# Performance work log

Measured on AMD Instinct MI355X. Metric: run time of the kernel, lower is better.

The kernel has to match this reference:

```python
import jax, jax.numpy as jnp
import numpy as np

B, S, D, H = 2, 2048, 1024, 16
HD = D // H
EPS = 1e-5

def _ln(x, g, b):
    mu = jnp.mean(x, axis=-1, keepdims=True)
    var = jnp.var(x, axis=-1, keepdims=True)
    return (x - mu) * jax.lax.rsqrt(var + EPS) * g + b

def setup_inputs() -> dict:
    key = jax.random.key(0)
    ks = jax.random.split(key, 6)
    sc = lambda n: 1.0 / np.sqrt(n)
    return {
        "x": jax.random.normal(ks[0], (B, S, D), jnp.float32),
        "W_qkv": jax.random.normal(ks[1], (D, 3 * D), jnp.float32) * sc(D),
        "b_qkv": jnp.zeros((3 * D,), jnp.float32),
        "W_o": jax.random.normal(ks[2], (D, D), jnp.float32) * sc(D),
        "b_o": jnp.zeros((D,), jnp.float32),
        "W_fc": jax.random.normal(ks[3], (D, 4 * D), jnp.float32) * sc(D),
        "b_fc": jnp.zeros((4 * D,), jnp.float32),
        "W_pr": jax.random.normal(ks[4], (4 * D, D), jnp.float32) * sc(4 * D),
        "b_pr": jnp.zeros((D,), jnp.float32),
        "g1": jnp.ones((D,), jnp.float32),
        "beta1": jnp.zeros((D,), jnp.float32),
        "g2": jnp.ones((D,), jnp.float32),
        "beta2": jnp.zeros((D,), jnp.float32),
    }

def reference(x, W_qkv, b_qkv, W_o, b_o, W_fc, b_fc, W_pr, b_pr, g1, beta1, g2, beta2):
    # pre-norm attention
    h = _ln(x, g1, beta1)
    qkv = h @ W_qkv + b_qkv                      # [B,S,3D]
    q, k, v = jnp.split(qkv, 3, axis=-1)
    q = q.reshape(B, S, H, HD).transpose(0, 2, 1, 3)  # [B,H,S,hd]
    k = k.reshape(B, S, H, HD).transpose(0, 2, 1, 3)
    v = v.reshape(B, S, H, HD).transpose(0, 2, 1, 3)
    scores = jnp.einsum('bhqd,bhkd->bhqk', q, k) / np.sqrt(HD)
    causal = jnp.tril(jnp.ones((S, S), bool))
    scores = jnp.where(causal, scores, -jnp.inf)
    attn = jax.nn.softmax(scores, axis=-1)
    out = jnp.einsum('bhqk,bhkd->bhqd', attn, v)
    out = out.transpose(0, 2, 1, 3).reshape(B, S, D)
    x = x + out @ W_o + b_o
    # pre-norm MLP (exact erf GELU, matching torch F.gelu default)
    h2 = _ln(x, g2, beta2)
    h2 = jax.nn.gelu(h2 @ W_fc + b_fc, approximate=False)
    x = x + h2 @ W_pr + b_pr
    return x
```

## Files before the change

### kernel.cpp

```cpp
#include <hip/hip_runtime.h>
#include <cstdint>
#include <cstddef>

#define Bb 2
#define Ss 2048
#define Dd 1024
#define Hh 16

typedef __attribute__((ext_vector_type(8))) short short8;
typedef __attribute__((ext_vector_type(4))) short short4v;
typedef __attribute__((ext_vector_type(4))) float float4v;

__device__ inline short f2bf(float f) {
  unsigned u = __builtin_bit_cast(unsigned, f);
  u = (u + 0x7fffu + ((u >> 16) & 1u)) >> 16;
  return (short)u;
}

__device__ inline float bf2f(short s) {
  unsigned u = ((unsigned)(unsigned short)s) << 16;
  return __builtin_bit_cast(float, u);
}

__device__ inline unsigned cvt_pk_bf16(float lo, float hi) {
  unsigned r;
  asm("v_cvt_pk_bf16_f32 %0, %1, %2" : "=v"(r) : "v"(lo), "v"(hi));
  return r;
}

__device__ inline void gl_lds16(const void* g, void* l) {
  __builtin_amdgcn_global_load_lds(
      (__attribute__((address_space(1))) void*)(void*)(g),
      (__attribute__((address_space(3))) void*)(l), 16, 0, 0);
}

#define MFMA(a, b, c) __builtin_amdgcn_mfma_f32_16x16x32_bf16((a), (b), (c), 0, 0, 0)

__device__ __forceinline__ void ln_row(const float* __restrict__ x,
                                       const float* __restrict__ g,
                                       const float* __restrict__ be,
                                       short* __restrict__ out, int row,
                                       float* red) {
  int tid = threadIdx.x;
  const float4* xr = (const float4*)(x + (size_t)row * Dd);
  float4 v = xr[tid];
  float s = v.x + v.y + v.z + v.w;
  float q = v.x * v.x + v.y * v.y + v.z * v.z + v.w * v.w;
#pragma unroll
  for (int off = 1; off < 64; off <<= 1) {
    s += __shfl_xor(s, off);
    q += __shfl_xor(q, off);
  }
  int w = tid >> 6;
  if ((tid & 63) == 0) { red[w] = s; red[4 + w] = q; }
  __syncthreads();
  s = red[0] + red[1] + red[2] + red[3];
  q = red[4] + red[5] + red[6] + red[7];
  float mu = s * (1.0f / Dd);
  float var = q * (1.0f / Dd) - mu * mu;
  float rstd = rsqrtf(var + 1e-5f);
  float4 gv = ((const float4*)g)[tid], bv = ((const float4*)be)[tid];
  short4v o;
  o.x = f2bf((v.x - mu) * rstd * gv.x + bv.x);
  o.y = f2bf((v.y - mu) * rstd * gv.y + bv.y);
  o.z = f2bf((v.z - mu) * rstd * gv.z + bv.z);
  o.w = f2bf((v.w - mu) * rstd * gv.w + bv.w);
  *(short4v*)(out + (size_t)row * Dd + tid * 4) = o;
}

__global__ __launch_bounds__(256) void prep_kernel(
    const float* __restrict__ W0, short* __restrict__ T0,
    const float* __restrict__ W1, short* __restrict__ T1,
    const float* __restrict__ W2, short* __restrict__ T2,
    const float* __restrict__ W3, short* __restrict__ T3,
    const float* __restrict__ x, const float* __restrict__ g1,
    const float* __restrict__ be1, short* __restrict__ h1) {
  __shared__ __align__(16) float t[32][33];
  int id = blockIdx.x;
  if (id >= 12288) {
    ln_row(x, g1, be1, h1, id - 12288, &t[0][0]);
    return;
  }
  const float* W; short* Wt; int N, K, tix;
  if (id < 3072)      { W = W0; Wt = T0; N = 3072; K = 1024; tix = id; }
  else if (id < 4096) { W = W1; Wt = T1; N = 1024; K = 1024; tix = id - 3072; }
  else if (id < 8192) { W = W2; Wt = T2; N = 4096; K = 1024; tix = id - 4096; }
  else                { W = W3; Wt = T3; N = 1024; K = 4096; tix = id - 8192; }
  int nx = N / 32;
  int n0 = (tix % nx) * 32, k0 = (tix / nx) * 32;
  int tx = threadIdx.x & 31, ty = threadIdx.x >> 5;
#pragma unroll
  for (int i = 0; i < 4; i++)
    t[ty + 8 * i][tx] = W[(size_t)(k0 + ty + 8 * i) * N + n0 + tx];
  __syncthreads();
#pragma unroll
  for (int i = 0; i < 4; i++)
    Wt[(size_t)(n0 + ty + 8 * i) * K + k0 + tx] = f2bf(t[tx][ty + 8 * i]);
}

__global__ __launch_bounds__(256) void reduce_ln_kernel(const float* __restrict__ x,
                                                        const float* __restrict__ bias,
                                                        const short* __restrict__ parts,
                                                        const float* __restrict__ g,
                                                        const float* __restrict__ be,
                                                        float* __restrict__ x1,
                                                        short* __restrict__ h2) {
  int row = blockIdx.x, tid = threadIdx.x;
  size_t base = (size_t)row * Dd + tid * 4;
  float4 v = *(const float4*)(x + base);
  float4 bv = ((const float4*)bias)[tid];
  v.x += bv.x; v.y += bv.y; v.z += bv.z; v.w += bv.w;
#pragma unroll
  for (int s = 0; s < 2; s++) {
    short4v p = *(const short4v*)(parts + (size_t)s * 4096 * Dd + base);
    v.x += bf2f(p.x); v.y += bf2f(p.y); v.z += bf2f(p.z); v.w += bf2f(p.w);
  }
  *(float4*)(x1 + base) = v;
  float s = v.x + v.y + v.z + v.w;
  float q = v.x * v.x + v.y * v.y + v.z * v.z + v.w * v.w;
#pragma unroll
  for (int off = 1; off < 64; off <<= 1) {
    s += __shfl_xor(s, off);
    q += __shfl_xor(q, off);
  }
  __shared__ float as_[4], aq_[4];
  int w = tid >> 6;
  if ((tid & 63) == 0) { as_[w] = s; aq_[w] = q; }
  __syncthreads();
  s = as_[0] + as_[1] + as_[2] + as_[3];
  q = aq_[0] + aq_[1] + aq_[2] + aq_[3];
  float mu = s * (1.0f / Dd);
  float var = q * (1.0f / Dd) - mu * mu;
  float rstd = rsqrtf(var + 1e-5f);
  float4 gv = ((const float4*)g)[tid], b2 = ((const float4*)be)[tid];
  short4v o;
  o.x = f2bf((v.x - mu) * rstd * gv.x + b2.x);
  o.y = f2bf((v.y - mu) * rstd * gv.y + b2.y);
  o.z = f2bf((v.z - mu) * rstd * gv.z + b2.z);
  o.w = f2bf((v.w - mu) * rstd * gv.w + b2.w);
  *(short4v*)(h2 + base) = o;
}

__global__ __launch_bounds__(256) void reduce_kernel(const float* __restrict__ src,
                                                     const float* __restrict__ bias,
                                                     const short* __restrict__ parts,
                                                     float* __restrict__ dst) {
  int row = blockIdx.x, tid = threadIdx.x;
  size_t base = (size_t)row * Dd + tid * 4;
  float4 v = *(const float4*)(src + base);
  float4 bv = ((const float4*)bias)[tid];
  v.x += bv.x; v.y += bv.y; v.z += bv.z; v.w += bv.w;
#pragma unroll
  for (int s = 0; s < 2; s++) {
    short4v p = *(const short4v*)(parts + (size_t)s * 4096 * Dd + base);
    v.x += bf2f(p.x); v.y += bf2f(p.y); v.z += bf2f(p.z); v.w += bf2f(p.w);
  }
  *(float4*)(dst + base) = v;
}

template <int MODE>
__device__ __forceinline__ void gemm_tile(const short* __restrict__ A,
                                          const short* __restrict__ Bt,
                                          const float* __restrict__ bias,
                                          void* __restrict__ outp,
                                          short* __restrict__ vtp,
                                          int M, int N, int K,
                                          int m0, int n0, int zp,
                                          int ks, int ke, char* smem) {
  short* As = (short*)smem;
  short* Bs = (short*)smem + 128 * 64;
  const int tid = threadIdx.x;
  const int w = tid >> 6, lane = tid & 63;
  const int sr = lane >> 3;
  const int sc = lane & 7;
  const int gc = sc ^ sr;
  const int fr = lane & 15;
  const int g = lane >> 4;
  const int wm = (w >> 1) * 64, wn = (w & 1) * 64;
  float4v acc[4][4] = {};
  const short* Ag = A + (size_t)(m0 + w * 32 + sr) * K + gc * 8;
  const short* Bg = Bt + (size_t)(n0 + w * 32 + sr) * K + gc * 8;
  short* Asw = As + (w * 32 + sr) * 64 + sc * 8;
  short* Bsw = Bs + (w * 32 + sr) * 64 + sc * 8;
#pragma unroll
  for (int i = 0; i < 4; i++) {
    gl_lds16(Ag + (size_t)(i * 8) * K + ks, Asw + i * 8 * 64);
    gl_lds16(Bg + (size_t)(i * 8) * K + ks, Bsw + i * 8 * 64);
  }
  for (int k0 = ks; k0 < ke; k0 += 64) {
    __syncthreads();
    short8 a[2][4], b[2][4];
#pragma unroll
    for (int kh = 0; kh < 2; kh++) {
#pragma unroll
      for (int i = 0; i < 4; i++) {
        int row = wm + i * 16 + fr;
        int slot = (g + kh * 4) ^ (row & 7);
        a[kh][i] = *(const short8*)(As + row * 64 + slot * 8);
      }
#pragma unroll
      for (int j = 0; j < 4; j++) {
        int row = wn + j * 16 + fr;
        int slot = (g + kh * 4) ^ (row & 7);
        b[kh][j] = *(const short8*)(Bs + row * 64 + slot * 8);
      }
    }
    __syncthreads();
    if (k0 + 64 < ke) {
#pragma unroll
      for (int i = 0; i < 4; i++) {
        gl_lds16(Ag + (size_t)(i * 8) * K + k0 + 64, Asw + i * 8 * 64);
        gl_lds16(Bg + (size_t)(i * 8) * K + k0 + 64, Bsw + i * 8 * 64);
      }
    }
#pragma unroll
    for (int kh = 0; kh < 2; kh++)
#pragma unroll
      for (int i = 0; i < 4; i++)
#pragma unroll
        for (int j = 0; j < 4; j++)
          acc[i][j] = MFMA(a[kh][i], b[kh][j], acc[i][j]);
  }
  const int crow = g * 4;
  const int ccol = fr;
#pragma unroll
  for (int i = 0; i < 4; i++) {
#pragma unroll
    for (int j = 0; j < 4; j++) {
      int col = n0 + wn + j * 16 + ccol;
      float bcol = (MODE == 3) ? 0.f : bias[col];
      short sh[4];
#pragma unroll
      for (int r = 0; r < 4; r++) {
        int row = m0 + wm + i * 16 + crow + r;
        float v = acc[i][j][r] + bcol;
        if (MODE == 4) {
          if (col < 1024) v *= 0.18033688f;
          sh[r] = f2bf(v);
          ((short*)outp)[(size_t)row * N + col] = sh[r];
        } else if (MODE == 2) {
          float y = 0.79788456f * (v + 0.044715f * v * v * v);
          float e = __builtin_amdgcn_exp2f(y * 2.885390082f);
          float th = 1.0f - 2.0f * __builtin_amdgcn_rcpf(e + 1.0f);
          v = 0.5f * v * (1.0f + th);
          ((short*)outp)[(size_t)row * N + col] = f2bf(v);
        } else {
          short* pp = (short*)outp + (size_t)zp * M * N;
          pp[(size_t)row * N + col] = f2bf(v);
        }
      }
      if (MODE == 4 && col >= 2048) {
        int hd = col - 2048;
        int rbase = m0 + wm + i * 16 + crow;
        int bq = rbase >> 11, sb = rbase & 2047;
        int bh = bq * 16 + (hd >> 6), d = hd & 63;
        short4v pk;
        pk.x = sh[0]; pk.y = sh[1]; pk.z = sh[2]; pk.w = sh[3];
        *(short4v*)(vtp + (size_t)(bh * 64 + d) * Ss + sb) = pk;
      }
    }
  }
}

__global__ __launch_bounds__(256) void k_gemm_qkv(const short* __restrict__ A,
                                                  const short* __restrict__ Bt,
                                                  const float* __restrict__ bias,
                                                  short* __restrict__ o,
                                                  short* __restrict__ Vt) {
  __shared__ __align__(16) char smem[32768];
  int t = blockIdx.x;
  int c8 = t & 7, tt = t >> 3;
  int m0 = ((c8 >> 1) * 8 + tt / 12) * 128;
  int n0 = ((c8 & 1) * 12 + tt % 12) * 128;
  gemm_tile<4>(A, Bt, bias, o, Vt, 4096, 3072, 1024, m0, n0, 0, 0, 1024, smem);
}

__global__ __launch_bounds__(256) void k_gemm_fc(const short* __restrict__ A,
                                                 const short* __restrict__ Bt,
                                                 const float* __restrict__ bias,
                                                 short* __restrict__ o) {
  __shared__ __align__(16) char smem[32768];
  int t = blockIdx.x;
  int c8 = t & 7, tt = t >> 3;
  int m0 = ((c8 >> 1) * 8 + tt / 16) * 128;
  int n0 = ((c8 & 1) * 16 + tt % 16) * 128;
  gemm_tile<2>(A, Bt, bias, o, nullptr, 4096, 4096, 1024, m0, n0, 0, 0, 1024, smem);
}

__global__ __launch_bounds__(256) void k_gemm_wo(const short* __restrict__ A,
                                                 const short* __restrict__ Bt,
                                                 short* __restrict__ parts) {
  __shared__ __align__(16) char smem[32768];
  int c = blockIdx.x;
  int z = c >> 8, rem = c & 255;
  int c8 = rem & 7, tt = rem >> 3;
  int m0 = (c8 * 4 + tt / 8) * 128, n0 = (tt % 8) * 128;
  gemm_tile<3>(A, Bt, nullptr, parts, nullptr, 4096, 1024, 1024, m0, n0, z,
               z * 512, z * 512 + 512, smem);
}

__global__ __launch_bounds__(256) void k_gemm_pr(const short* __restrict__ A,
                                                 const short* __restrict__ Bt,
                                                 short* __restrict__ parts) {
  __shared__ __align__(16) char smem[32768];
  int c = blockIdx.x;
  int z = c >> 8, rem = c & 255;
  int c8 = rem & 7, tt = rem >> 3;
  int m0 = (c8 * 4 + tt / 8) * 128, n0 = (tt % 8) * 128;
  gemm_tile<3>(A, Bt, nullptr, parts, nullptr, 4096, 1024, 4096, m0, n0, z,
               z * 2048, z * 2048 + 2048, smem);
}

__global__ __launch_bounds__(256) void flash_kernel(const short* __restrict__ qkv,
                                                    const short* __restrict__ Vt,
                                                    short* __restrict__ att) {
  __shared__ __align__(16) short Ks[4096];
  __shared__ __align__(16) short Vs[4096];
  __shared__ __align__(16) short P[4][16 * 72];
  const int w = threadIdx.x >> 6, lane = threadIdx.x & 63;
  const int qb = 31 - (blockIdx.x >> 5);
  const int bh = blockIdx.x & 31;
  const int b = bh >> 4, h = bh & 15;
  const int qbase = qb * 64 + w * 16;
  const int q = lane & 15;
  const int g = lane >> 4;
  const int fk = g * 8;
  short* Pw = &P[w][0];

  const int L0 = w * 64 + lane, L1 = L0 + 256;
  const int r0 = L0 >> 3, c0 = (L0 & 7) ^ (r0 & 7);
  const int r1 = L1 >> 3, c1 = (L1 & 7) ^ (r1 & 7);
  const short* kg0 = qkv + (size_t)(b * Ss + r0) * 3072 + 1024 + h * 64 + c0 * 8;
  const short* kg1 = qkv + (size_t)(b * Ss + r1) * 3072 + 1024 + h * 64 + c1 * 8;
  const short* vg0 = Vt + (size_t)(bh * 64 + r0) * Ss + c0 * 8;
  const short* vg1 = Vt + (size_t)(bh * 64 + r1) * Ss + c1 * 8;

  short8 qf[2];
  {
    const short* qrow = qkv + (size_t)(b * Ss + qbase + q) * 3072 + h * 64;
    qf[0] = *(const short8*)(qrow + fk);
    qf[1] = *(const short8*)(qrow + 32 + fk);
  }
  float4v o[4] = {};
  float l_i = 0.f;
  const int nkt = qb + 1;

  gl_lds16(kg0, Ks + L0 * 8);
  gl_lds16(kg1, Ks + L1 * 8);
  gl_lds16(vg0, Vs + L0 * 8);
  gl_lds16(vg1, Vs + L1 * 8);

  for (int kt = 0; kt < nkt; kt++) {
    const int kbase = kt * 64;
    __syncthreads();

    short8 kf[4][2], vf[4][2];
#pragma unroll
    for (int t = 0; t < 4; t++) {
      const int row = 16 * t + q;
      const int sw = (g ^ (row & 7)) * 8;
      kf[t][0] = *(const short8*)(Ks + row * 64 + sw);
      kf[t][1] = *(const short8*)(Ks + row * 64 + (sw ^ 32));
      vf[t][0] = *(const short8*)(Vs + row * 64 + sw);
      vf[t][1] = *(const short8*)(Vs + row * 64 + (sw ^ 32));
    }
    __syncthreads();
    if (kt + 1 < nkt) {
      const size_t nb = (size_t)(kbase + 64);
      gl_lds16(kg0 + nb * 3072, Ks + L0 * 8);
      gl_lds16(kg1 + nb * 3072, Ks + L1 * 8);
      gl_lds16(vg0 + nb, Vs + L0 * 8);
      gl_lds16(vg1 + nb, Vs + L1 * 8);
    }

    float4v s[4] = {};
#pragma unroll
    for (int t = 0; t < 4; t++) {
      s[t] = MFMA(kf[t][0], qf[0], s[t]);
      s[t] = MFMA(kf[t][1], qf[1], s[t]);
    }
    const bool maskt = (kbase + 63 > qbase);
    const int qlim = qbase + q - kbase;
    float p[4][4];
    float rs = 0.f;
#pragma unroll
    for (int t = 0; t < 4; t++) {
#pragma unroll
      for (int r = 0; r < 4; r++) {
        float v = s[t][r];
        if (maskt && (16 * t + 4 * g + r > qlim)) v = -3.0e38f;
        float e = __builtin_amdgcn_exp2f(v);
        p[t][r] = e;
        rs += e;
      }
    }
    rs += __shfl_xor(rs, 16);
    rs += __shfl_xor(rs, 32);
    l_i += rs;
#pragma unroll
    for (int t = 0; t < 4; t++) {
      uint2 u;
      u.x = cvt_pk_bf16(p[t][0], p[t][1]);
      u.y = cvt_pk_bf16(p[t][2], p[t][3]);
      *(uint2*)(Pw + q * 72 + 16 * t + 4 * g) = u;
    }
    asm volatile("s_waitcnt lgkmcnt(0)" ::: "memory");
    short8 pb0 = *(const short8*)(Pw + q * 72 + fk);
    short8 pb1 = *(const short8*)(Pw + q * 72 + 32 + fk);
#pragma unroll
    for (int t = 0; t < 4; t++) {
      o[t] = MFMA(vf[t][0], pb0, o[t]);
      o[t] = MFMA(vf[t][1], pb1, o[t]);
    }
  }
  const float inv = 1.0f / l_i;
  const int orow = b * Ss + qbase + q;
#pragma unroll
  for (int t = 0; t < 4; t++) {
    uint2 ov;
    ov.x = cvt_pk_bf16(o[t][0] * inv, o[t][1] * inv);
    ov.y = cvt_pk_bf16(o[t][2] * inv, o[t][3] * inv);
    *(uint2*)(att + (size_t)orow * Dd + h * 64 + 16 * t + 4 * g) = ov;
  }
}

extern "C" void kernel_launch(void* const* d_in, const int* in_sizes, int n_in,
                              void* d_out, int out_size, void* d_ws, size_t ws_size,
                              hipStream_t stream) {
  const float* x    = (const float*)d_in[0];
  const float* Wqkv = (const float*)d_in[1];
  const float* bqkv = (const float*)d_in[2];
  const float* Wo   = (const float*)d_in[3];
  const float* bo   = (const float*)d_in[4];
  const float* Wfc  = (const float*)d_in[5];
  const float* bfc  = (const float*)d_in[6];
  const float* Wpr  = (const float*)d_in[7];
  const float* bpr  = (const float*)d_in[8];
  const float* g1   = (const float*)d_in[9];
  const float* be1  = (const float*)d_in[10];
  const float* g2   = (const float*)d_in[11];
  const float* be2  = (const float*)d_in[12];

  char* ws = (char*)d_ws;
  const size_t MB = 1024 * 1024;
  short* h1     = (short*)(ws + 0);
  short* qkvb   = (short*)(ws + 8 * MB);
  short* partWo = (short*)(ws + 0);
  short* partPr = (short*)(ws + 0);
  short* Vt     = (short*)(ws + 32 * MB);
  short* att    = (short*)(ws + 40 * MB);
  float* x1     = (float*)(ws + 48 * MB);
  short* h2     = (short*)(ws + 64 * MB);
  short* geluo  = (short*)(ws + 72 * MB);
  short* WtQkv  = (short*)(ws + 104 * MB);
  short* WtO    = (short*)(ws + 110 * MB);
  short* WtFc   = (short*)(ws + 112 * MB);
  short* WtPr   = (short*)(ws + 120 * MB);

  prep_kernel<<<16384, 256, 0, stream>>>(Wqkv, WtQkv, Wo, WtO, Wfc, WtFc,
                                         Wpr, WtPr, x, g1, be1, h1);
  k_gemm_qkv<<<768, 256, 0, stream>>>(h1, WtQkv, bqkv, qkvb, Vt);
  flash_kernel<<<1024, 256, 0, stream>>>(qkvb, Vt, att);
  k_gemm_wo<<<512, 256, 0, stream>>>(att, WtO, partWo);
  reduce_ln_kernel<<<4096, 256, 0, stream>>>(x, bo, partWo, g2, be2, x1, h2);
  k_gemm_fc<<<1024, 256, 0, stream>>>(h2, WtFc, bfc, geluo);
  k_gemm_pr<<<512, 256, 0, stream>>>(geluo, WtPr, partPr);
  reduce_kernel<<<4096, 256, 0, stream>>>(x1, bpr, partPr, (float*)d_out);
}
```

Measured before the change: 307.0 us.

## Enlarge weight-transpose tiles and widen flash attention blocks to 128 queries

The weight transpose/convert kernel now uses 64x64 tiles per block instead of 32x32, cutting the block count and giving each block more work. The flash attention kernel now runs 8 waves covering 128 query rows, so each K/V tile loaded into LDS is shared by twice as many queries. Each block now loads only one 16-byte chunk of K and one of V per thread. Waves whose queries sit entirely before the current key tile skip compute but still join the barriers. This halves K/V global traffic for attention at the cost of more causal imbalance inside a block, a larger LDS footprint, and fewer blocks.

```diff
diff --git a/kernel.cpp b/kernel.cpp
--- a/kernel.cpp
+++ b/kernel.cpp
@@ -75,27 +75,27 @@
     const float* __restrict__ W3, short* __restrict__ T3,
     const float* __restrict__ x, const float* __restrict__ g1,
     const float* __restrict__ be1, short* __restrict__ h1) {
-  __shared__ __align__(16) float t[32][33];
+  __shared__ __align__(16) float t[64][65];
   int id = blockIdx.x;
-  if (id >= 12288) {
-    ln_row(x, g1, be1, h1, id - 12288, &t[0][0]);
+  if (id >= 3072) {
+    ln_row(x, g1, be1, h1, id - 3072, &t[0][0]);
     return;
   }
   const float* W; short* Wt; int N, K, tix;
-  if (id < 3072)      { W = W0; Wt = T0; N = 3072; K = 1024; tix = id; }
-  else if (id < 4096) { W = W1; Wt = T1; N = 1024; K = 1024; tix = id - 3072; }
-  else if (id < 8192) { W = W2; Wt = T2; N = 4096; K = 1024; tix = id - 4096; }
-  else                { W = W3; Wt = T3; N = 1024; K = 4096; tix = id - 8192; }
-  int nx = N / 32;
-  int n0 = (tix % nx) * 32, k0 = (tix / nx) * 32;
-  int tx = threadIdx.x & 31, ty = threadIdx.x >> 5;
-#pragma unroll
-  for (int i = 0; i < 4; i++)
-    t[ty + 8 * i][tx] = W[(size_t)(k0 + ty + 8 * i) * N + n0 + tx];
+  if (id < 768)       { W = W0; Wt = T0; N = 3072; K = 1024; tix = id; }
+  else if (id < 1024) { W = W1; Wt = T1; N = 1024; K = 1024; tix = id - 768; }
+  else if (id < 2048) { W = W2; Wt = T2; N = 4096; K = 1024; tix = id - 1024; }
+  else                { W = W3; Wt = T3; N = 1024; K = 4096; tix = id - 2048; }
+  int nx = N / 64;
+  int n0 = (tix % nx) * 64, k0 = (tix / nx) * 64;
+  int tx = threadIdx.x & 63, ty = threadIdx.x >> 6;
+#pragma unroll
+  for (int i = 0; i < 16; i++)
+    t[ty + 4 * i][tx] = W[(size_t)(k0 + ty + 4 * i) * N + n0 + tx];
   __syncthreads();
 #pragma unroll
-  for (int i = 0; i < 4; i++)
-    Wt[(size_t)(n0 + ty + 8 * i) * K + k0 + tx] = f2bf(t[tx][ty + 8 * i]);
+  for (int i = 0; i < 16; i++)
+    Wt[(size_t)(n0 + ty + 4 * i) * K + k0 + tx] = f2bf(t[tx][ty + 4 * i]);
 }
 
 __global__ __launch_bounds__(256) void reduce_ln_kernel(const float* __restrict__ x,
@@ -311,29 +311,28 @@
                z * 2048, z * 2048 + 2048, smem);
 }
 
-__global__ __launch_bounds__(256) void flash_kernel(const short* __restrict__ qkv,
+__global__ __launch_bounds__(512) void flash_kernel(const short* __restrict__ qkv,
                                                     const short* __restrict__ Vt,
                                                     short* __restrict__ att) {
   __shared__ __align__(16) short Ks[4096];
   __shared__ __align__(16) short Vs[4096];
-  __shared__ __align__(16) short P[4][16 * 72];
-  const int w = threadIdx.x >> 6, lane = threadIdx.x & 63;
-  const int qb = 31 - (blockIdx.x >> 5);
-  const int bh = blockIdx.x & 31;
+  __shared__ __align__(16) short P[8][16 * 72];
+  const int tid = threadIdx.x;
+  const int w = tid >> 6, lane = tid & 63;
+  const int bidx = blockIdx.x;
+  const int bh = bidx & 31;
+  const int hv = bidx >> 5;
+  const int qb = (bidx < 256) ? (15 - hv) : (hv - 8);
   const int b = bh >> 4, h = bh & 15;
-  const int qbase = qb * 64 + w * 16;
+  const int qbase = qb * 128 + w * 16;
   const int q = lane & 15;
   const int g = lane >> 4;
   const int fk = g * 8;
   short* Pw = &P[w][0];
 
-  const int L0 = w * 64 + lane, L1 = L0 + 256;
-  const int r0 = L0 >> 3, c0 = (L0 & 7) ^ (r0 & 7);
-  const int r1 = L1 >> 3, c1 = (L1 & 7) ^ (r1 & 7);
+  const int r0 = tid >> 3, c0 = (tid & 7) ^ (r0 & 7);
   const short* kg0 = qkv + (size_t)(b * Ss + r0) * 3072 + 1024 + h * 64 + c0 * 8;
-  const short* kg1 = qkv + (size_t)(b * Ss + r1) * 3072 + 1024 + h * 64 + c1 * 8;
   const short* vg0 = Vt + (size_t)(bh * 64 + r0) * Ss + c0 * 8;
-  const short* vg1 = Vt + (size_t)(bh * 64 + r1) * Ss + c1 * 8;
 
   short8 qf[2];
   {
@@ -343,35 +342,35 @@
   }
   float4v o[4] = {};
   float l_i = 0.f;
-  const int nkt = qb + 1;
-
-  gl_lds16(kg0, Ks + L0 * 8);
-  gl_lds16(kg1, Ks + L1 * 8);
-  gl_lds16(vg0, Vs + L0 * 8);
-  gl_lds16(vg1, Vs + L1 * 8);
+  const int nkt = 2 * qb + 2;
+
+  gl_lds16(kg0, Ks + tid * 8);
+  gl_lds16(vg0, Vs + tid * 8);
 
   for (int kt = 0; kt < nkt; kt++) {
     const int kbase = kt * 64;
+    const bool active = (kbase <= qbase + 15);
     __syncthreads();
 
     short8 kf[4][2], vf[4][2];
-#pragma unroll
-    for (int t = 0; t < 4; t++) {
-      const int row = 16 * t + q;
-      const int sw = (g ^ (row & 7)) * 8;
-      kf[t][0] = *(const short8*)(Ks + row * 64 + sw);
-      kf[t][1] = *(const short8*)(Ks + row * 64 + (sw ^ 32));
-      vf[t][0] = *(const short8*)(Vs + row * 64 + sw);
-      vf[t][1] = *(const short8*)(Vs + row * 64 + (sw ^ 32));
+    if (active) {
+#pragma unroll
+      for (int t = 0; t < 4; t++) {
+        const int row = 16 * t + q;
+        const int sw = (g ^ (row & 7)) * 8;
+        kf[t][0] = *(const short8*)(Ks + row * 64 + sw);
+        kf[t][1] = *(const short8*)(Ks + row * 64 + (sw ^ 32));
+        vf[t][0] = *(const short8*)(Vs + row * 64 + sw);
+        vf[t][1] = *(const short8*)(Vs + row * 64 + (sw ^ 32));
+      }
     }
     __syncthreads();
     if (kt + 1 < nkt) {
       const size_t nb = (size_t)(kbase + 64);
-      gl_lds16(kg0 + nb * 3072, Ks + L0 * 8);
-      gl_lds16(kg1 + nb * 3072, Ks + L1 * 8);
-      gl_lds16(vg0 + nb, Vs + L0 * 8);
-      gl_lds16(vg1 + nb, Vs + L1 * 8);
-    }
+      gl_lds16(kg0 + nb * 3072, Ks + tid * 8);
+      gl_lds16(vg0 + nb, Vs + tid * 8);
+    }
+    if (!active) continue;
 
     float4v s[4] = {};
 #pragma unroll
@@ -457,10 +456,10 @@
   short* WtFc   = (short*)(ws + 112 * MB);
   short* WtPr   = (short*)(ws + 120 * MB);
 
-  prep_kernel<<<16384, 256, 0, stream>>>(Wqkv, WtQkv, Wo, WtO, Wfc, WtFc,
-                                         Wpr, WtPr, x, g1, be1, h1);
+  prep_kernel<<<7168, 256, 0, stream>>>(Wqkv, WtQkv, Wo, WtO, Wfc, WtFc,
+                                        Wpr, WtPr, x, g1, be1, h1);
   k_gemm_qkv<<<768, 256, 0, stream>>>(h1, WtQkv, bqkv, qkvb, Vt);
-  flash_kernel<<<1024, 256, 0, stream>>>(qkvb, Vt, att);
+  flash_kernel<<<512, 512, 0, stream>>>(qkvb, Vt, att);
   k_gemm_wo<<<512, 256, 0, stream>>>(att, WtO, partWo);
   reduce_ln_kernel<<<4096, 256, 0, stream>>>(x, bo, partWo, g2, be2, x1, h2);
   k_gemm_fc<<<1024, 256, 0, stream>>>(h2, WtFc, bfc, geluo);
```

After: 313.7 us. +2.2%, slower.
